# Performance work log

Hardware: AMD Instinct MI355X
Metric: run time of the kernel (lower is better)

The kernel has to match this reference:

```python
import jax, jax.numpy as jnp
import numpy as np

B, T, C, H = 8, 2048, 1024, 64  # batch, seq (== block_size), n_embd, head_size


def setup_inputs() -> dict:
    key = jax.random.key(0)
    k1, k2, k3, k4 = jax.random.split(key, 4)
    x = jax.random.normal(k1, (B, T, C), dtype=jnp.float32)
    scale = 0.02
    Wk = jax.random.normal(k2, (H, C), dtype=jnp.float32) * scale  # nn.Linear weight [out,in]
    Wq = jax.random.normal(k3, (H, C), dtype=jnp.float32) * scale
    Wv = jax.random.normal(k4, (H, C), dtype=jnp.float32) * scale
    return {"x": x, "Wk": Wk, "Wq": Wq, "Wv": Wv}


def reference(x, Wk, Wq, Wv):
    # k, q, v projections (bias-free linears): x @ W.T
    k = jnp.einsum('btc,hc->bth', x, Wk)
    q = jnp.einsum('btc,hc->bth', x, Wq)
    v = jnp.einsum('btc,hc->bth', x, Wv)
    # NOTE: source MULTIPLIES by sqrt(head_size) (faithful to original code)
    wei = jnp.einsum('bth,bsh->bts', q, k) * (H ** 0.5)  # [B,T,T]
    causal = jnp.tril(jnp.ones((T, T), dtype=bool))
    wei = jnp.where(causal, wei, -jnp.inf)
    wei = jax.nn.softmax(wei, axis=-1)
    # dropout_value = 0.0 -> identity (deterministic baseline)
    out = jnp.einsum('bts,bsh->bth', wei, v)  # [B,T,H]
    return out
```

## Files before the change

kernel.cpp:

```cpp
#include <hip/hip_runtime.h>

#define BB 8
#define TT 2048
#define CC 1024
#define HH 64
#define MM (BB * TT)

typedef _Float16 half8 __attribute__((ext_vector_type(8)));
typedef _Float16 half4 __attribute__((ext_vector_type(4)));
typedef float floatx4 __attribute__((ext_vector_type(4)));

template <int CTRL>
__device__ __forceinline__ float dpp_max_step(float x)
{
    union { float f; int i; } u, v;
    u.f = x;
    v.i = __builtin_amdgcn_update_dpp(u.i, u.i, CTRL, 0xf, 0xf, false);
    return fmaxf(x, v.f);
}
__device__ __forceinline__ float rowmax16(float x)
{
    x = dpp_max_step<0x128>(x);
    x = dpp_max_step<0x124>(x);
    x = dpp_max_step<0x122>(x);
    x = dpp_max_step<0x121>(x);
    return x;
}

__global__ __launch_bounds__(256)
void w_pack(const float* __restrict__ Wk, const float* __restrict__ Wq,
            const float* __restrict__ Wv, _Float16* __restrict__ Wp)
{
    const int idx = (blockIdx.x * 256 + threadIdx.x) * 8;
    const int c   = idx / 6144;
    const int rm  = idx - c * 6144;
    const int row = rm >> 5;
    const int kk  = rm & 31;
    const int which = row >> 6;
    const float* __restrict__ src = (which == 0) ? Wq : ((which == 1) ? Wk : Wv);
    const float scale = (which == 0) ? 8.0f : 1.0f;
    const int srow = row & 63;
    const int k = c * 32 + kk;
    const float4 a = *reinterpret_cast<const float4*>(&src[srow * 1024 + k]);
    const float4 b = *reinterpret_cast<const float4*>(&src[srow * 1024 + k + 4]);
    const half8 o = { (_Float16)(a.x * scale), (_Float16)(a.y * scale),
                      (_Float16)(a.z * scale), (_Float16)(a.w * scale),
                      (_Float16)(b.x * scale), (_Float16)(b.y * scale),
                      (_Float16)(b.z * scale), (_Float16)(b.w * scale) };
    *reinterpret_cast<half8*>(&Wp[idx]) = o;
}

__global__ __launch_bounds__(64, 2)
void qkv7(const float* __restrict__ x, const _Float16* __restrict__ Wp,
          _Float16* __restrict__ q16, _Float16* __restrict__ Kp,
          _Float16* __restrict__ Vp)
{
    const int lane  = threadIdx.x;
    const int gw    = blockIdx.x;
    const int mtile = gw >> 1;
    const int nh    = gw & 1;
    const int m_base = mtile * 16;
    const int fm = lane & 15;
    const int fq = lane >> 4;
    const int fk = fq * 8;
    const int fr = fq * 4;

    const float*    __restrict__ xrow = &x[(size_t)(m_base + fm) * CC + fk];
    const _Float16* __restrict__ wb   = &Wp[(nh * 96 + fm) * 32 + fk];

    floatx4 acc[6];
    #pragma unroll
    for (int n = 0; n < 6; ++n)
        #pragma unroll
        for (int r = 0; r < 4; ++r) acc[n][r] = 0.0f;

    float4 xa, xb, nxa, nxb;
    half8 wf[6], nwf[6];

    xa = *reinterpret_cast<const float4*>(xrow);
    xb = *reinterpret_cast<const float4*>(xrow + 4);
    #pragma unroll
    for (int n = 0; n < 6; ++n)
        wf[n] = *reinterpret_cast<const half8*>(wb + n * 512);

    #pragma unroll 2
    for (int c = 0; c < 32; ++c) {
        if (c < 31) {
            const float* xp = xrow + (c + 1) * 32;
            nxa = *reinterpret_cast<const float4*>(xp);
            nxb = *reinterpret_cast<const float4*>(xp + 4);
            const _Float16* wc = wb + (c + 1) * 6144;
            #pragma unroll
            for (int n = 0; n < 6; ++n)
                nwf[n] = *reinterpret_cast<const half8*>(wc + n * 512);
        }
        const half8 af = { (_Float16)xa.x, (_Float16)xa.y, (_Float16)xa.z, (_Float16)xa.w,
                           (_Float16)xb.x, (_Float16)xb.y, (_Float16)xb.z, (_Float16)xb.w };
        #pragma unroll
        for (int n = 0; n < 6; ++n)
            acc[n] = __builtin_amdgcn_mfma_f32_16x16x32_f16(af, wf[n], acc[n], 0, 0, 0);
        xa = nxa; xb = nxb;
        #pragma unroll
        for (int n = 0; n < 6; ++n) wf[n] = nwf[n];
    }

    #pragma unroll
    for (int n = 0; n < 6; ++n) {
        const int col = nh * 96 + n * 16 + fm;
        if (col < 64) {
            #pragma unroll
            for (int r = 0; r < 4; ++r)
                q16[(size_t)(m_base + fr + r) * HH + col] = (_Float16)acc[n][r];
        } else if (col < 128) {
            const int h = col - 64;
            _Float16* kp = &Kp[(size_t)(mtile * 2 + (h >> 5)) * 512 + (h & 31)];
            #pragma unroll
            for (int r = 0; r < 4; ++r)
                kp[(fr + r) * 32] = (_Float16)acc[n][r];
        } else {
            const int h = col - 128;
            const half4 pk = { (_Float16)acc[n][0], (_Float16)acc[n][1],
                               (_Float16)acc[n][2], (_Float16)acc[n][3] };
            *reinterpret_cast<half4*>(
                &Vp[(size_t)((mtile >> 2) * 4 + (h >> 4)) * 1024 +
                    ((mtile >> 1) & 1) * 512 + fm * 32 + (mtile & 1) * 16 + fr]) = pk;
        }
    }
}

__global__ __launch_bounds__(64, 4)
void attn7(const _Float16* __restrict__ q16, const _Float16* __restrict__ Kp,
           const _Float16* __restrict__ Vp, float* __restrict__ out,
           _Float16* __restrict__ Op, float* __restrict__ ml)
{
    __shared__ _Float16 Ps[16 * 68];

    const int bid = blockIdx.x;
    const int it  = 127 - bid / 24;
    const int sub = bid - (127 - it) * 24;
    const int b   = sub & 7;
    const int s   = sub >> 3;

    const int lane = threadIdx.x;
    const int fm = lane & 15;
    const int fq = lane >> 4;
    const int fk = fq * 8;
    const int fr = fq * 4;

    const int Ji = (it >> 2) + 1;
    const int qq = Ji / 3, rem = Ji - qq * 3;
    const int cnt   = qq + (s < rem ? 1 : 0);
    const int start = s * qq + (s < rem ? s : rem);

    const _Float16* __restrict__ kpb = Kp + (size_t)b * TT * HH;
    const _Float16* __restrict__ vpb = Vp + (size_t)b * TT * HH;

    const int qrow = (b * 128 + it) * 16 + fm;
    const half8 qf0 = *reinterpret_cast<const half8*>(&q16[(size_t)qrow * HH + fk]);
    const half8 qf1 = *reinterpret_cast<const half8*>(&q16[(size_t)qrow * HH + 32 + fk]);

    floatx4 O[4], lacc;
    float m_r[4];
    #pragma unroll
    for (int r = 0; r < 4; ++r) {
        m_r[r] = -3.0e38f;
        lacc[r] = 0.0f;
        #pragma unroll
        for (int ht = 0; ht < 4; ++ht) O[ht][r] = 0.0f;
    }
    const half8 ones = { (_Float16)1.f, (_Float16)1.f, (_Float16)1.f, (_Float16)1.f,
                         (_Float16)1.f, (_Float16)1.f, (_Float16)1.f, (_Float16)1.f };

    const int loff = fm * 32 + fk;

    for (int js = 0; js < cnt; ++js) {
        const int jj = start + js;

        floatx4 sa[4];
        #pragma unroll
        for (int nt = 0; nt < 4; ++nt) {
            #pragma unroll
            for (int r = 0; r < 4; ++r) sa[nt][r] = 0.0f;
            const _Float16* kp = &kpb[(size_t)(jj * 4 + nt) * 1024];
            const half8 b0 = *reinterpret_cast<const half8*>(kp + loff);
            const half8 b1 = *reinterpret_cast<const half8*>(kp + 512 + loff);
            sa[nt] = __builtin_amdgcn_mfma_f32_16x16x32_f16(qf0, b0, sa[nt], 0, 0, 0);
            sa[nt] = __builtin_amdgcn_mfma_f32_16x16x32_f16(qf1, b1, sa[nt], 0, 0, 0);
        }

        if (jj == (it >> 2)) {
            const int rbase = it * 16 + fr;
            #pragma unroll
            for (int nt = 0; nt < 4; ++nt) {
                const int col = jj * 64 + nt * 16 + fm;
                #pragma unroll
                for (int r = 0; r < 4; ++r)
                    if (col > rbase + r) sa[nt][r] = -3.0e38f;
            }
        }

        #pragma unroll
        for (int r = 0; r < 4; ++r) {
            float mx = fmaxf(fmaxf(sa[0][r], sa[1][r]), fmaxf(sa[2][r], sa[3][r]));
            mx = rowmax16(mx);
            const float mn = fmaxf(m_r[r], mx);
            const float alpha = __expf(m_r[r] - mn);
            m_r[r] = mn;
            _Float16* pp = &Ps[(fr + r) * 68 + fm];
            pp[0]  = (_Float16)__expf(sa[0][r] - mn);
            pp[16] = (_Float16)__expf(sa[1][r] - mn);
            pp[32] = (_Float16)__expf(sa[2][r] - mn);
            pp[48] = (_Float16)__expf(sa[3][r] - mn);
            lacc[r] *= alpha;
            O[0][r] *= alpha; O[1][r] *= alpha; O[2][r] *= alpha; O[3][r] *= alpha;
        }

        #pragma unroll
        for (int ch = 0; ch < 2; ++ch) {
            const half8 pa = *reinterpret_cast<const half8*>(&Ps[fm * 68 + ch * 32 + fk]);
            lacc = __builtin_amdgcn_mfma_f32_16x16x32_f16(pa, ones, lacc, 0, 0, 0);
            #pragma unroll
            for (int ht = 0; ht < 4; ++ht) {
                const half8 vb = *reinterpret_cast<const half8*>(
                    &vpb[(size_t)(jj * 4 + ht) * 1024 + ch * 512 + loff]);
                O[ht] = __builtin_amdgcn_mfma_f32_16x16x32_f16(pa, vb, O[ht], 0, 0, 0);
            }
        }
    }

    #pragma unroll
    for (int r = 0; r < 4; ++r) {
        const int grow = (b * 128 + it) * 16 + fr + r;
        if (s == 0) {
            #pragma unroll
            for (int ht = 0; ht < 4; ++ht)
                out[(size_t)grow * HH + ht * 16 + fm] = O[ht][r];
        } else {
            #pragma unroll
            for (int ht = 0; ht < 4; ++ht)
                Op[((size_t)(s - 1) * MM + grow) * HH + ht * 16 + fm] = (_Float16)O[ht][r];
        }
        if (fm == 0) {
            ml[((size_t)s * MM + grow) * 2 + 0] = m_r[r];
            ml[((size_t)s * MM + grow) * 2 + 1] = lacc[r];
        }
    }
}

__global__ __launch_bounds__(256)
void combine(float* __restrict__ out, const _Float16* __restrict__ Op,
             const float* __restrict__ ml)
{
    const int tid  = threadIdx.x;
    const int grow = blockIdx.x * 64 + (tid >> 2);
    const int c0   = (tid & 3) * 16;

    const float m0 = ml[(size_t)grow * 2 + 0];
    const float l0 = ml[(size_t)grow * 2 + 1];
    const float m1 = ml[((size_t)MM + grow) * 2 + 0];
    const float l1 = ml[((size_t)MM + grow) * 2 + 1];
    const float m2 = ml[((size_t)2 * MM + grow) * 2 + 0];
    const float l2 = ml[((size_t)2 * MM + grow) * 2 + 1];

    const float M  = fmaxf(m0, fmaxf(m1, m2));
    const float w0 = __expf(m0 - M);
    const float w1 = __expf(m1 - M);
    const float w2 = __expf(m2 - M);
    const float inv = 1.0f / (w0 * l0 + w1 * l1 + w2 * l2);

    #pragma unroll
    for (int i = 0; i < 16; i += 4) {
        float4 o0 = *reinterpret_cast<float4*>(&out[(size_t)grow * HH + c0 + i]);
        const half4 h1 = *reinterpret_cast<const half4*>(&Op[(size_t)grow * HH + c0 + i]);
        const half4 h2 = *reinterpret_cast<const half4*>(&Op[(size_t)MM * HH + (size_t)grow * HH + c0 + i]);
        o0.x = (w0 * o0.x + w1 * (float)h1[0] + w2 * (float)h2[0]) * inv;
        o0.y = (w0 * o0.y + w1 * (float)h1[1] + w2 * (float)h2[1]) * inv;
        o0.z = (w0 * o0.z + w1 * (float)h1[2] + w2 * (float)h2[2]) * inv;
        o0.w = (w0 * o0.w + w1 * (float)h1[3] + w2 * (float)h2[3]) * inv;
        *reinterpret_cast<float4*>(&out[(size_t)grow * HH + c0 + i]) = o0;
    }
}

extern "C" void kernel_launch(void* const* d_in, const int* in_sizes, int n_in,
                              void* d_out, int out_size, void* d_ws, size_t ws_size,
                              hipStream_t stream)
{
    (void)in_sizes; (void)n_in; (void)out_size; (void)ws_size;

    const float* x  = (const float*)d_in[0];
    const float* Wk = (const float*)d_in[1];
    const float* Wq = (const float*)d_in[2];
    const float* Wv = (const float*)d_in[3];
    float* out = (float*)d_out;

    _Float16* base = (_Float16*)d_ws;
    _Float16* q16 = base;
    _Float16* Kp  = base + (size_t)MM * HH;
    _Float16* Vp  = base + (size_t)2 * MM * HH;
    _Float16* Wp  = base + (size_t)3 * MM * HH;
    _Float16* Op  = Wp + 192 * 1024;
    float*    ml  = (float*)(Op + (size_t)2 * MM * HH);

    w_pack<<<dim3(96), dim3(256), 0, stream>>>(Wk, Wq, Wv, Wp);
    qkv7<<<dim3(2048), dim3(64), 0, stream>>>(x, Wp, q16, Kp, Vp);
    attn7<<<dim3(3072), dim3(64), 0, stream>>>(q16, Kp, Vp, out, Op, ml);
    combine<<<dim3(256), dim3(256), 0, stream>>>(out, Op, ml);
}
```

Baseline: 152.7 us.

## Split QKV projection into four column groups with double-buffered loads

The QKV projection kernel now splits the 192 output columns into four groups of 48 instead of two of 96, launching 4096 single-wave blocks with higher launch-bounds occupancy. It also replaces the unrolled prefetch loop with an explicit two-stage register double buffer. Each block holds fewer accumulators, which should raise occupancy and latency hiding. The cost is that each x row tile is re-read by four blocks instead of two, doubling x global traffic (mostly served by cache).

```diff
diff --git a/kernel.cpp b/kernel.cpp
--- a/kernel.cpp
+++ b/kernel.cpp
@@ -50,15 +50,15 @@
     *reinterpret_cast<half8*>(&Wp[idx]) = o;
 }
 
-__global__ __launch_bounds__(64, 2)
-void qkv7(const float* __restrict__ x, const _Float16* __restrict__ Wp,
+__global__ __launch_bounds__(64, 4)
+void qkv8(const float* __restrict__ x, const _Float16* __restrict__ Wp,
           _Float16* __restrict__ q16, _Float16* __restrict__ Kp,
           _Float16* __restrict__ Vp)
 {
     const int lane  = threadIdx.x;
     const int gw    = blockIdx.x;
-    const int mtile = gw >> 1;
-    const int nh    = gw & 1;
+    const int mtile = gw & 1023;
+    const int nq    = gw >> 10;
     const int m_base = mtile * 16;
     const int fm = lane & 15;
     const int fq = lane >> 4;
@@ -66,47 +66,80 @@
     const int fr = fq * 4;
 
     const float*    __restrict__ xrow = &x[(size_t)(m_base + fm) * CC + fk];
-    const _Float16* __restrict__ wb   = &Wp[(nh * 96 + fm) * 32 + fk];
-
-    floatx4 acc[6];
-    #pragma unroll
-    for (int n = 0; n < 6; ++n)
+    const _Float16* __restrict__ wb   = &Wp[(nq * 48 + fm) * 32 + fk];
+
+    floatx4 acc[3];
+    #pragma unroll
+    for (int n = 0; n < 3; ++n)
         #pragma unroll
         for (int r = 0; r < 4; ++r) acc[n][r] = 0.0f;
 
-    float4 xa, xb, nxa, nxb;
-    half8 wf[6], nwf[6];
-
-    xa = *reinterpret_cast<const float4*>(xrow);
-    xb = *reinterpret_cast<const float4*>(xrow + 4);
-    #pragma unroll
-    for (int n = 0; n < 6; ++n)
-        wf[n] = *reinterpret_cast<const half8*>(wb + n * 512);
-
-    #pragma unroll 2
-    for (int c = 0; c < 32; ++c) {
-        if (c < 31) {
-            const float* xp = xrow + (c + 1) * 32;
-            nxa = *reinterpret_cast<const float4*>(xp);
-            nxb = *reinterpret_cast<const float4*>(xp + 4);
-            const _Float16* wc = wb + (c + 1) * 6144;
-            #pragma unroll
-            for (int n = 0; n < 6; ++n)
-                nwf[n] = *reinterpret_cast<const half8*>(wc + n * 512);
-        }
-        const half8 af = { (_Float16)xa.x, (_Float16)xa.y, (_Float16)xa.z, (_Float16)xa.w,
-                           (_Float16)xb.x, (_Float16)xb.y, (_Float16)xb.z, (_Float16)xb.w };
-        #pragma unroll
-        for (int n = 0; n < 6; ++n)
-            acc[n] = __builtin_amdgcn_mfma_f32_16x16x32_f16(af, wf[n], acc[n], 0, 0, 0);
-        xa = nxa; xb = nxb;
-        #pragma unroll
-        for (int n = 0; n < 6; ++n) wf[n] = nwf[n];
-    }
-
-    #pragma unroll
-    for (int n = 0; n < 6; ++n) {
-        const int col = nh * 96 + n * 16 + fm;
+    float4 xa0, xb0, xa1, xb1;
+    half8 w0[3], w1[3];
+
+    xa0 = *reinterpret_cast<const float4*>(xrow);
+    xb0 = *reinterpret_cast<const float4*>(xrow + 4);
+    xa1 = *reinterpret_cast<const float4*>(xrow + 32);
+    xb1 = *reinterpret_cast<const float4*>(xrow + 36);
+    #pragma unroll
+    for (int n = 0; n < 3; ++n) {
+        w0[n] = *reinterpret_cast<const half8*>(wb + n * 512);
+        w1[n] = *reinterpret_cast<const half8*>(wb + 6144 + n * 512);
+    }
+
+    for (int cc = 0; cc < 15; ++cc) {
+        const int c0 = cc * 2;
+        {
+            const half8 af = { (_Float16)xa0.x, (_Float16)xa0.y, (_Float16)xa0.z, (_Float16)xa0.w,
+                               (_Float16)xb0.x, (_Float16)xb0.y, (_Float16)xb0.z, (_Float16)xb0.w };
+            #pragma unroll
+            for (int n = 0; n < 3; ++n)
+                acc[n] = __builtin_amdgcn_mfma_f32_16x16x32_f16(af, w0[n], acc[n], 0, 0, 0);
+        }
+        {
+            const float* xp = xrow + (c0 + 2) * 32;
+            xa0 = *reinterpret_cast<const float4*>(xp);
+            xb0 = *reinterpret_cast<const float4*>(xp + 4);
+            const _Float16* wc = wb + (size_t)(c0 + 2) * 6144;
+            #pragma unroll
+            for (int n = 0; n < 3; ++n)
+                w0[n] = *reinterpret_cast<const half8*>(wc + n * 512);
+        }
+        {
+            const half8 af = { (_Float16)xa1.x, (_Float16)xa1.y, (_Float16)xa1.z, (_Float16)xa1.w,
+                               (_Float16)xb1.x, (_Float16)xb1.y, (_Float16)xb1.z, (_Float16)xb1.w };
+            #pragma unroll
+            for (int n = 0; n < 3; ++n)
+                acc[n] = __builtin_amdgcn_mfma_f32_16x16x32_f16(af, w1[n], acc[n], 0, 0, 0);
+        }
+        {
+            const float* xp = xrow + (c0 + 3) * 32;
+            xa1 = *reinterpret_cast<const float4*>(xp);
+            xb1 = *reinterpret_cast<const float4*>(xp + 4);
+            const _Float16* wc = wb + (size_t)(c0 + 3) * 6144;
+            #pragma unroll
+            for (int n = 0; n < 3; ++n)
+                w1[n] = *reinterpret_cast<const half8*>(wc + n * 512);
+        }
+    }
+    {
+        const half8 af = { (_Float16)xa0.x, (_Float16)xa0.y, (_Float16)xa0.z, (_Float16)xa0.w,
+                           (_Float16)xb0.x, (_Float16)xb0.y, (_Float16)xb0.z, (_Float16)xb0.w };
+        #pragma unroll
+        for (int n = 0; n < 3; ++n)
+            acc[n] = __builtin_amdgcn_mfma_f32_16x16x32_f16(af, w0[n], acc[n], 0, 0, 0);
+    }
+    {
+        const half8 af = { (_Float16)xa1.x, (_Float16)xa1.y, (_Float16)xa1.z, (_Float16)xa1.w,
+                           (_Float16)xb1.x, (_Float16)xb1.y, (_Float16)xb1.z, (_Float16)xb1.w };
+        #pragma unroll
+        for (int n = 0; n < 3; ++n)
+            acc[n] = __builtin_amdgcn_mfma_f32_16x16x32_f16(af, w1[n], acc[n], 0, 0, 0);
+    }
+
+    #pragma unroll
+    for (int n = 0; n < 3; ++n) {
+        const int col = nq * 48 + n * 16 + fm;
         if (col < 64) {
             #pragma unroll
             for (int r = 0; r < 4; ++r)
@@ -302,7 +335,7 @@
     float*    ml  = (float*)(Op + (size_t)2 * MM * HH);
 
     w_pack<<<dim3(96), dim3(256), 0, stream>>>(Wk, Wq, Wv, Wp);
-    qkv7<<<dim3(2048), dim3(64), 0, stream>>>(x, Wp, q16, Kp, Vp);
+    qkv8<<<dim3(4096), dim3(64), 0, stream>>>(x, Wp, q16, Kp, Vp);
     attn7<<<dim3(3072), dim3(64), 0, stream>>>(q16, Kp, Vp, out, Op, ml);
     combine<<<dim3(256), dim3(256), 0, stream>>>(out, Op, ml);
 }
```

Measured after the change: 166.4 us. 9.0% more time.

## Restructure QKV projection into 512-thread blocks with LDS-staged x via async loads

Applied to the files above, without the earlier changes.

Replaces the one-wave-per-tile QKV projection with 8-wave blocks that each cover 64 rows. The x tile is staged in LDS through a 4-deep ring filled by global_load_lds, with an XOR swizzle against bank conflicts. Before, each x row was loaded from global memory by two separate waves (one per column half); now it is loaded once and shared by the four waves that split the 192 output columns. The cost is a block barrier every k-step and the hand-written vmcnt waits, which must match the number of loads in flight.

```diff
diff --git a/kernel.cpp b/kernel.cpp
--- a/kernel.cpp
+++ b/kernel.cpp
@@ -26,6 +26,15 @@
     x = dpp_max_step<0x121>(x);
     return x;
 }
+
+__device__ __forceinline__ void gll16(const float* g, float* l)
+{
+    __builtin_amdgcn_global_load_lds(
+        (const __attribute__((address_space(1))) unsigned int*)g,
+        (__attribute__((address_space(3))) unsigned int*)l, 16, 0, 0);
+}
+
+#define MEMFENCE asm volatile("" ::: "memory")
 
 __global__ __launch_bounds__(256)
 void w_pack(const float* __restrict__ Wk, const float* __restrict__ Wq,
@@ -50,80 +59,119 @@
     *reinterpret_cast<half8*>(&Wp[idx]) = o;
 }
 
-__global__ __launch_bounds__(64, 2)
-void qkv7(const float* __restrict__ x, const _Float16* __restrict__ Wp,
+__global__ __launch_bounds__(512, 2)
+void qkv9(const float* __restrict__ x, const _Float16* __restrict__ Wp,
           _Float16* __restrict__ q16, _Float16* __restrict__ Kp,
           _Float16* __restrict__ Vp)
 {
-    const int lane  = threadIdx.x;
-    const int gw    = blockIdx.x;
-    const int mtile = gw >> 1;
-    const int nh    = gw & 1;
-    const int m_base = mtile * 16;
+    __shared__ float xs[4][64][32];
+
+    const int tid  = threadIdx.x;
+    const int lane = tid & 63;
+    const int w    = tid >> 6;
+    const int blk  = blockIdx.x;
+    const int m_base = blk * 64;
     const int fm = lane & 15;
     const int fq = lane >> 4;
     const int fk = fq * 8;
     const int fr = fq * 4;
-
-    const float*    __restrict__ xrow = &x[(size_t)(m_base + fm) * CC + fk];
-    const _Float16* __restrict__ wb   = &Wp[(nh * 96 + fm) * 32 + fk];
-
-    floatx4 acc[6];
-    #pragma unroll
-    for (int n = 0; n < 6; ++n)
-        #pragma unroll
-        for (int r = 0; r < 4; ++r) acc[n][r] = 0.0f;
-
-    float4 xa, xb, nxa, nxb;
-    half8 wf[6], nwf[6];
-
-    xa = *reinterpret_cast<const float4*>(xrow);
-    xb = *reinterpret_cast<const float4*>(xrow + 4);
-    #pragma unroll
-    for (int n = 0; n < 6; ++n)
-        wf[n] = *reinterpret_cast<const half8*>(wb + n * 512);
-
-    #pragma unroll 2
-    for (int c = 0; c < 32; ++c) {
-        if (c < 31) {
-            const float* xp = xrow + (c + 1) * 32;
-            nxa = *reinterpret_cast<const float4*>(xp);
-            nxb = *reinterpret_cast<const float4*>(xp + 4);
-            const _Float16* wc = wb + (c + 1) * 6144;
-            #pragma unroll
-            for (int n = 0; n < 6; ++n)
-                nwf[n] = *reinterpret_cast<const half8*>(wc + n * 512);
-        }
-        const half8 af = { (_Float16)xa.x, (_Float16)xa.y, (_Float16)xa.z, (_Float16)xa.w,
-                           (_Float16)xb.x, (_Float16)xb.y, (_Float16)xb.z, (_Float16)xb.w };
-        #pragma unroll
-        for (int n = 0; n < 6; ++n)
-            acc[n] = __builtin_amdgcn_mfma_f32_16x16x32_f16(af, wf[n], acc[n], 0, 0, 0);
-        xa = nxa; xb = nxb;
-        #pragma unroll
-        for (int n = 0; n < 6; ++n) wf[n] = nwf[n];
-    }
-
-    #pragma unroll
-    for (int n = 0; n < 6; ++n) {
-        const int col = nh * 96 + n * 16 + fm;
-        if (col < 64) {
-            #pragma unroll
-            for (int r = 0; r < 4; ++r)
-                q16[(size_t)(m_base + fr + r) * HH + col] = (_Float16)acc[n][r];
-        } else if (col < 128) {
-            const int h = col - 64;
-            _Float16* kp = &Kp[(size_t)(mtile * 2 + (h >> 5)) * 512 + (h & 31)];
-            #pragma unroll
-            for (int r = 0; r < 4; ++r)
-                kp[(fr + r) * 32] = (_Float16)acc[n][r];
-        } else {
-            const int h = col - 128;
-            const half4 pk = { (_Float16)acc[n][0], (_Float16)acc[n][1],
-                               (_Float16)acc[n][2], (_Float16)acc[n][3] };
-            *reinterpret_cast<half4*>(
-                &Vp[(size_t)((mtile >> 2) * 4 + (h >> 4)) * 1024 +
-                    ((mtile >> 1) & 1) * 512 + fm * 32 + (mtile & 1) * 16 + fr]) = pk;
+    const int wm = w >> 2;
+    const int wn = w & 3;
+
+    const float* gsrc = &x[(size_t)(m_base + w * 8 + (lane >> 3)) * CC
+                           + ((lane & 7) ^ (lane >> 3)) * 4];
+    float* ldst = &xs[0][w * 8][0];
+
+    const _Float16* wb = &Wp[(wn * 48 + fm) * 32 + fk];
+
+    floatx4 acc[2][3];
+    #pragma unroll
+    for (int a = 0; a < 2; ++a)
+        #pragma unroll
+        for (int n = 0; n < 3; ++n)
+            #pragma unroll
+            for (int r = 0; r < 4; ++r) acc[a][n][r] = 0.0f;
+
+    half8 wA[3], wB[3];
+
+    #pragma unroll
+    for (int n = 0; n < 3; ++n)
+        wA[n] = *reinterpret_cast<const half8*>(wb + n * 512);
+    MEMFENCE;
+    gll16(gsrc + 0 * 32, ldst + 0 * 2048);
+    gll16(gsrc + 1 * 32, ldst + 1 * 2048);
+    gll16(gsrc + 2 * 32, ldst + 2 * 2048);
+    asm volatile("s_waitcnt vmcnt(2)" ::: "memory");
+    __builtin_amdgcn_s_barrier();
+    MEMFENCE;
+
+#define QKV_ITER(c, WUSE, WLOAD, DO_W, DO_X, NWAIT)                            \
+    {                                                                          \
+        if (DO_W) {                                                            \
+            _Pragma("unroll")                                                  \
+            for (int n = 0; n < 3; ++n)                                        \
+                WLOAD[n] = *reinterpret_cast<const half8*>(                    \
+                    wb + (size_t)((c) + 1) * 6144 + n * 512);                  \
+        }                                                                      \
+        MEMFENCE;                                                              \
+        if (DO_X) gll16(gsrc + ((c) + 3) * 32, ldst + (((c) + 3) & 3) * 2048); \
+        _Pragma("unroll")                                                      \
+        for (int a = 0; a < 2; ++a) {                                          \
+            const int rr = wm * 32 + a * 16 + fm;                              \
+            const float* rowp = &xs[(c) & 3][rr][0];                           \
+            const int sw = fm & 7;                                             \
+            const float4 v0 = *reinterpret_cast<const float4*>(                \
+                rowp + ((fq * 2 + 0) ^ sw) * 4);                               \
+            const float4 v1 = *reinterpret_cast<const float4*>(                \
+                rowp + ((fq * 2 + 1) ^ sw) * 4);                               \
+            const half8 af = { (_Float16)v0.x, (_Float16)v0.y,                 \
+                               (_Float16)v0.z, (_Float16)v0.w,                 \
+                               (_Float16)v1.x, (_Float16)v1.y,                 \
+                               (_Float16)v1.z, (_Float16)v1.w };               \
+            _Pragma("unroll")                                                  \
+            for (int n = 0; n < 3; ++n)                                        \
+                acc[a][n] = __builtin_amdgcn_mfma_f32_16x16x32_f16(            \
+                    af, WUSE[n], acc[a][n], 0, 0, 0);                          \
+        }                                                                      \
+        asm volatile("s_waitcnt vmcnt(" #NWAIT ")" ::: "memory");              \
+        __builtin_amdgcn_s_barrier();                                          \
+        MEMFENCE;                                                              \
+    }
+
+    for (int cc = 0; cc < 28; cc += 2) {
+        QKV_ITER(cc,     wA, wB, true,  true,  8);
+        QKV_ITER(cc + 1, wB, wA, true,  true,  8);
+    }
+    QKV_ITER(28, wA, wB, true,  true,  8);
+    QKV_ITER(29, wB, wA, true,  false, 4);
+    QKV_ITER(30, wA, wB, true,  false, 0);
+    QKV_ITER(31, wB, wA, false, false, 0);
+#undef QKV_ITER
+
+    #pragma unroll
+    for (int a = 0; a < 2; ++a) {
+        const int mt = blk * 4 + wm * 2 + a;
+        #pragma unroll
+        for (int n = 0; n < 3; ++n) {
+            const int col = wn * 48 + n * 16 + fm;
+            if (col < 64) {
+                #pragma unroll
+                for (int r = 0; r < 4; ++r)
+                    q16[(size_t)(mt * 16 + fr + r) * HH + col] = (_Float16)acc[a][n][r];
+            } else if (col < 128) {
+                const int h = col - 64;
+                _Float16* kp = &Kp[(size_t)(mt * 2 + (h >> 5)) * 512 + (h & 31)];
+                #pragma unroll
+                for (int r = 0; r < 4; ++r)
+                    kp[(fr + r) * 32] = (_Float16)acc[a][n][r];
+            } else {
+                const int h = col - 128;
+                const half4 pk = { (_Float16)acc[a][n][0], (_Float16)acc[a][n][1],
+                                   (_Float16)acc[a][n][2], (_Float16)acc[a][n][3] };
+                *reinterpret_cast<half4*>(
+                    &Vp[(size_t)((mt >> 2) * 4 + (h >> 4)) * 1024 +
+                        ((mt >> 1) & 1) * 512 + fm * 32 + (mt & 1) * 16 + fr]) = pk;
+            }
         }
     }
 }
@@ -302,7 +350,7 @@
     float*    ml  = (float*)(Op + (size_t)2 * MM * HH);
 
     w_pack<<<dim3(96), dim3(256), 0, stream>>>(Wk, Wq, Wv, Wp);
-    qkv7<<<dim3(2048), dim3(64), 0, stream>>>(x, Wp, q16, Kp, Vp);
+    qkv9<<<dim3(256), dim3(512), 0, stream>>>(x, Wp, q16, Kp, Vp);
     attn7<<<dim3(3072), dim3(64), 0, stream>>>(q16, Kp, Vp, out, Op, ml);
     combine<<<dim3(256), dim3(256), 0, stream>>>(out, Op, ml);
 }
```

New measurement: 151.0 us. Within noise of the previous version (-1.1%).
